# Performance work log

Hardware: AMD Instinct MI355X
Metric: run time of the kernel (lower is better)

## Reference

```python
import jax, jax.numpy as jnp
import numpy as np

N_EXPERTS = 8
TOP_K = 2

def setup_inputs() -> dict:
    key = jax.random.key(0)
    k1, k2, k3, k4 = jax.random.split(key, 4)
    B, T, C, F, E = 4, 1024, 1024, 2048, N_EXPERTS
    x = jax.random.normal(k1, (B, T, C), dtype=jnp.float32)
    router_w = jax.random.normal(k2, (E, C), dtype=jnp.float32) * 0.02
    w_v = jax.random.normal(k3, (E, C, 2 * F), dtype=jnp.float32) * 0.02
    c_proj = jax.random.normal(k4, (E, F, C), dtype=jnp.float32) * 0.02
    return {"x": x, "router_w": router_w, "w_v": w_v, "c_proj": c_proj}

def reference(x, router_w, w_v, c_proj):
    B, T, C = x.shape
    E = router_w.shape[0]
    # Router: top-k softmax
    logits = jnp.einsum('btc,ec->bte', x, router_w)
    probs = jax.nn.softmax(logits, axis=-1)
    weights, indices = jax.lax.top_k(probs, TOP_K)          # [B,T,K]
    weights = weights / jnp.sum(weights, axis=-1, keepdims=True)
    avg_probs = jnp.mean(probs, axis=(0, 1))
    aux_loss = E * jnp.sum(avg_probs * avg_probs)
    # Dense per-expert SwiGLU MLP on all tokens (idiomatic jax MoE reference)
    xf = x.reshape(B * T, C)                                # [N,C]
    h = jnp.einsum('nc,ecf->enf', xf, w_v)                  # [E,N,2F]
    gate, value = jnp.split(h, 2, axis=-1)
    act = jax.nn.silu(gate) * value                         # [E,N,F]
    eo = jnp.einsum('enf,efc->nec', act, c_proj)            # [N,E,C]
    # Combine: gather each token's top-k expert outputs and weight-sum
    idx = indices.reshape(B * T, TOP_K)                     # [N,K]
    w = weights.reshape(B * T, TOP_K)                       # [N,K]
    sel = jnp.take_along_axis(eo, idx[:, :, None], axis=1)  # [N,K,C]
    out = jnp.sum(w[:, :, None] * sel, axis=1)              # [N,C]
    return out.reshape(B, T, C), aux_loss
```

## Files before the change

kernel.cpp:

```cpp
#include <hip/hip_runtime.h>
#include <hip/hip_bf16.h>
#include <stdint.h>

#define N_TOK 4096
#define C_DIM 1024
#define F_DIM 2048
#define E_NUM 8
#define SMAX 9216
#define TILES_MAX 72
#define RBLK 1024

typedef __attribute__((ext_vector_type(4))) float f32x4;
typedef __attribute__((ext_vector_type(8))) short s16x8;

__device__ __forceinline__ uint16_t f2bf(float f) {
    unsigned x;
    __builtin_memcpy(&x, &f, 4);
    unsigned r = (x + 0x7fffu + ((x >> 16) & 1u)) >> 16;
    return (uint16_t)r;
}
__device__ __forceinline__ float bf2f(uint16_t u) {
    unsigned v = (unsigned)u << 16;
    float f;
    __builtin_memcpy(&f, &v, 4);
    return f;
}

#define GLL16(gp, lp)                                                                  \
    __builtin_amdgcn_global_load_lds((const __attribute__((address_space(1))) unsigned int*)(gp), \
                                     (__attribute__((address_space(3))) unsigned int*)(lp), 16, 0, 0)

__global__ void router_kernel(const float* __restrict__ x, const float* __restrict__ rw,
                              int* __restrict__ topk_idx, float* __restrict__ topk_w,
                              float* __restrict__ psum_part, int* __restrict__ cnt_part) {
    __shared__ float s_p[E_NUM];
    __shared__ int s_c[E_NUM];
    if (threadIdx.x < E_NUM) { s_p[threadIdx.x] = 0.f; s_c[threadIdx.x] = 0; }
    __syncthreads();

    int lane = threadIdx.x & 63;
    int wv = threadIdx.x >> 6;
    int t = blockIdx.x * 4 + wv;

    const float* xr = x + (size_t)t * C_DIM + lane * 16;
    float xs[16];
    for (int i = 0; i < 4; i++) *(float4*)&xs[i * 4] = *(const float4*)(xr + i * 4);

    float acc[E_NUM];
    for (int e = 0; e < E_NUM; e++) {
        const float* wr = rw + e * C_DIM + lane * 16;
        float s = 0.f;
        for (int i = 0; i < 4; i++) {
            float4 v = *(const float4*)(wr + i * 4);
            s += xs[i * 4] * v.x + xs[i * 4 + 1] * v.y + xs[i * 4 + 2] * v.z + xs[i * 4 + 3] * v.w;
        }
        acc[e] = s;
    }
    for (int off = 32; off > 0; off >>= 1)
        for (int e = 0; e < E_NUM; e++) acc[e] += __shfl_down(acc[e], off, 64);

    if (lane == 0) {
        float m = acc[0];
        for (int e = 1; e < E_NUM; e++) m = fmaxf(m, acc[e]);
        float p[E_NUM], s = 0.f;
        for (int e = 0; e < E_NUM; e++) { p[e] = __expf(acc[e] - m); s += p[e]; }
        float inv = 1.f / s;
        for (int e = 0; e < E_NUM; e++) { p[e] *= inv; atomicAdd(&s_p[e], p[e]); }
        int i0 = 0;
        for (int e = 1; e < E_NUM; e++) if (p[e] > p[i0]) i0 = e;
        int i1 = (i0 == 0) ? 1 : 0;
        for (int e = 0; e < E_NUM; e++) if (e != i0 && p[e] > p[i1]) i1 = e;
        float w0 = p[i0], w1 = p[i1], wsum = w0 + w1;
        topk_idx[t * 2] = i0; topk_idx[t * 2 + 1] = i1;
        topk_w[t * 2] = w0 / wsum; topk_w[t * 2 + 1] = w1 / wsum;
        atomicAdd(&s_c[i0], 1); atomicAdd(&s_c[i1], 1);
    }
    __syncthreads();
    if (threadIdx.x < E_NUM) {
        psum_part[blockIdx.x * E_NUM + threadIdx.x] = s_p[threadIdx.x];
        cnt_part[blockIdx.x * E_NUM + threadIdx.x] = s_c[threadIdx.x];
    }
}

__global__ void reduce_plan_kernel(const float* __restrict__ psum_part, const int* __restrict__ cnt_part,
                                   int* __restrict__ offsets, int* __restrict__ tile_expert,
                                   int* __restrict__ tile_row0, float* __restrict__ aux_out) {
    __shared__ float sp[256];
    __shared__ int sc[256];
    __shared__ int s_count[E_NUM];
    __shared__ float s_psum[E_NUM];
    int e = threadIdx.x >> 5, i = threadIdx.x & 31;
    float fp = 0.f; int c = 0;
    for (int j = i; j < RBLK; j += 32) { fp += psum_part[j * E_NUM + e]; c += cnt_part[j * E_NUM + e]; }
    sp[threadIdx.x] = fp; sc[threadIdx.x] = c;
    __syncthreads();
    for (int s = 16; s > 0; s >>= 1) {
        if (i < s) { sp[threadIdx.x] += sp[threadIdx.x + s]; sc[threadIdx.x] += sc[threadIdx.x + s]; }
        __syncthreads();
    }
    if (i == 0) { s_count[e] = sc[threadIdx.x]; s_psum[e] = sp[threadIdx.x]; }
    __syncthreads();
    if (threadIdx.x == 0) {
        int off = 0, t = 0;
        for (int ee = 0; ee < E_NUM; ee++) {
            offsets[ee] = off;
            int n = s_count[ee];
            int nt = (n + 127) >> 7;
            for (int k = 0; k < nt; k++) { tile_expert[t] = ee; tile_row0[t] = off + k * 128; t++; }
            off += nt * 128;
        }
        offsets[E_NUM] = off;
        for (; t < TILES_MAX; t++) tile_expert[t] = -1;
        float s = 0.f;
        for (int ee = 0; ee < E_NUM; ee++) { float a = s_psum[ee] * (1.f / N_TOK); s += a * a; }
        aux_out[0] = 8.f * s;
    }
}

__global__ void assign_kernel(const int* __restrict__ topk_idx, const float* __restrict__ topk_w,
                              const int* __restrict__ offsets, int* __restrict__ count2,
                              int* __restrict__ slot_map, float* __restrict__ slot_w,
                              int* __restrict__ tok_slot) {
    __shared__ int h[E_NUM];
    __shared__ int base[E_NUM];
    if (threadIdx.x < E_NUM) h[threadIdx.x] = 0;
    __syncthreads();
    int item = blockIdx.x * 256 + threadIdx.x;
    int e = topk_idx[item];
    int rank = atomicAdd(&h[e], 1);
    __syncthreads();
    if (threadIdx.x < E_NUM)
        base[threadIdx.x] = offsets[threadIdx.x] + atomicAdd(&count2[threadIdx.x], h[threadIdx.x]);
    __syncthreads();
    int slot = base[e] + rank;
    slot_map[slot] = item;
    slot_w[slot] = topk_w[item];
    tok_slot[item] = slot;
}

__global__ void gather_kernel(const float* __restrict__ x, const int* __restrict__ slot_map,
                              uint16_t* __restrict__ x_slots) {
    int slot = blockIdx.x;
    int item = slot_map[slot];
    if (item < 0) return;
    int t = item >> 1;
    float4 v = *(const float4*)(x + (size_t)t * C_DIM + threadIdx.x * 4);
    union { uint16_t u[4]; uint2 q; } r;
    r.u[0] = f2bf(v.x); r.u[1] = f2bf(v.y); r.u[2] = f2bf(v.z); r.u[3] = f2bf(v.w);
    *(uint2*)(x_slots + (size_t)slot * C_DIM + threadIdx.x * 4) = r.q;
}

__global__ __launch_bounds__(256) void convT_kernel(const float* __restrict__ in,
                                                    uint16_t* __restrict__ out, int R, int Cc) {
    __shared__ uint16_t s[128 * 66];
    size_t zb = (size_t)blockIdx.z * (size_t)R * Cc;
    int c0 = blockIdx.x * 64, r0 = blockIdx.y * 128;
    int cx = (threadIdx.x & 15) * 4, ry = threadIdx.x >> 4;
    for (int j = 0; j < 8; j++) {
        int r = ry + j * 16;
        float4 v = *(const float4*)(in + zb + (size_t)(r0 + r) * Cc + c0 + cx);
        uint16_t* p = &s[r * 66 + cx];
        p[0] = f2bf(v.x); p[1] = f2bf(v.y); p[2] = f2bf(v.z); p[3] = f2bf(v.w);
    }
    __syncthreads();
    int oc = threadIdx.x & 63, wseg = threadIdx.x >> 6;
    uint16_t tmp[32];
    for (int j = 0; j < 32; j++) tmp[j] = s[(wseg * 32 + j) * 66 + oc];
    uint4* dst = (uint4*)(out + zb + (size_t)(c0 + oc) * R + r0 + wseg * 32);
    dst[0] = *(const uint4*)&tmp[0];
    dst[1] = *(const uint4*)&tmp[8];
    dst[2] = *(const uint4*)&tmp[16];
    dst[3] = *(const uint4*)&tmp[24];
}


__global__ __launch_bounds__(256) void gemm1_kernel(const uint16_t* __restrict__ x_slots,
                                                    const uint16_t* __restrict__ wvT,
                                                    const int* __restrict__ tile_expert,
                                                    const int* __restrict__ tile_row0,
                                                    uint16_t* __restrict__ act) {
    int e = tile_expert[blockIdx.y];
    if (e < 0) return;
    int row0 = tile_row0[blockIdx.y];
    int j = blockIdx.x;
    __shared__ uint16_t As[128 * 32];
    __shared__ uint16_t Bg[64 * 32];
    __shared__ uint16_t Bv[64 * 32];
    int lane = threadIdx.x & 63, w = threadIdx.x >> 6;
    int wm = w & 1, wn = w >> 1;
    const uint16_t* wvb = wvT + (size_t)e * 4096 * 1024;

    int sk = (((lane & 3) ^ ((lane >> 3) & 3))) * 8;
    int ar = w * 32 + (lane >> 2);
    const uint16_t* agp0 = x_slots + (size_t)(row0 + ar) * C_DIM + sk;
    const uint16_t* agp1 = agp0 + (size_t)16 * C_DIM;
    int br = w * 16 + (lane >> 2);
    const uint16_t* bgp = wvb + (size_t)(j * 64 + br) * C_DIM + sk;
    const uint16_t* bvp = wvb + (size_t)(2048 + j * 64 + br) * C_DIM + sk;

    int cswz = ((lane >> 4) ^ ((lane >> 1) & 3)) * 8;

    f32x4 accg[4][2], accv[4][2];
    f32x4 z4 = {0.f, 0.f, 0.f, 0.f};
    for (int mf = 0; mf < 4; mf++)
        for (int nf = 0; nf < 2; nf++) { accg[mf][nf] = z4; accv[mf][nf] = z4; }

    for (int kt = 0; kt < 32; ++kt) {
        int ko = kt * 32;
        __syncthreads();
        GLL16(agp0 + ko, As + w * 1024);
        GLL16(agp1 + ko, As + w * 1024 + 512);
        GLL16(bgp + ko, Bg + w * 512);
        GLL16(bvp + ko, Bv + w * 512);
        __syncthreads();
        s16x8 af[4], bg[2], bv[2];
        for (int mf = 0; mf < 4; mf++)
            af[mf] = *(const s16x8*)&As[(wm * 64 + mf * 16 + (lane & 15)) * 32 + cswz];
        for (int nf = 0; nf < 2; nf++) {
            bg[nf] = *(const s16x8*)&Bg[(wn * 32 + nf * 16 + (lane & 15)) * 32 + cswz];
            bv[nf] = *(const s16x8*)&Bv[(wn * 32 + nf * 16 + (lane & 15)) * 32 + cswz];
        }
        for (int mf = 0; mf < 4; mf++)
            for (int nf = 0; nf < 2; nf++) {
                accg[mf][nf] = __builtin_amdgcn_mfma_f32_16x16x32_bf16(af[mf], bg[nf], accg[mf][nf], 0, 0, 0);
                accv[mf][nf] = __builtin_amdgcn_mfma_f32_16x16x32_bf16(af[mf], bv[nf], accv[mf][nf], 0, 0, 0);
            }
    }
    for (int mf = 0; mf < 4; mf++)
        for (int nf = 0; nf < 2; nf++)
            for (int r = 0; r < 4; r++) {
                int row = row0 + wm * 64 + mf * 16 + (lane >> 4) * 4 + r;
                int col = j * 64 + wn * 32 + nf * 16 + (lane & 15);
                float g = accg[mf][nf][r], v = accv[mf][nf][r];
                float a = g * v / (1.f + __expf(-g));
                act[(size_t)row * F_DIM + col] = f2bf(a);
            }
}

__global__ __launch_bounds__(256) void gemm2_kernel(const uint16_t* __restrict__ act,
                                                    const uint16_t* __restrict__ cpT,
                                                    const int* __restrict__ tile_expert,
                                                    const int* __restrict__ tile_row0,
                                                    const int* __restrict__ slot_map,
                                                    const float* __restrict__ slot_w,
                                                    uint16_t* __restrict__ eo) {
    int e = tile_expert[blockIdx.y];
    if (e < 0) return;
    int row0 = tile_row0[blockIdx.y];
    int cb = blockIdx.x * 128;
    __shared__ uint16_t As[128 * 32];
    __shared__ uint16_t Bs[128 * 32];
    int lane = threadIdx.x & 63, w = threadIdx.x >> 6;
    int wm = w & 1, wn = w >> 1;
    const uint16_t* cpb = cpT + (size_t)e * 1024 * 2048;

    int sk = (((lane & 3) ^ ((lane >> 3) & 3))) * 8;
    int ar = w * 32 + (lane >> 2);
    const uint16_t* agp0 = act + (size_t)(row0 + ar) * F_DIM + sk;
    const uint16_t* agp1 = agp0 + (size_t)16 * F_DIM;
    const uint16_t* bgp0 = cpb + (size_t)(cb + ar) * F_DIM + sk;
    const uint16_t* bgp1 = bgp0 + (size_t)16 * F_DIM;

    int cswz = ((lane >> 4) ^ ((lane >> 1) & 3)) * 8;

    f32x4 acc[4][4];
    f32x4 z4 = {0.f, 0.f, 0.f, 0.f};
    for (int mf = 0; mf < 4; mf++)
        for (int nf = 0; nf < 4; nf++) acc[mf][nf] = z4;

    for (int kt = 0; kt < 64; ++kt) {
        int ko = kt * 32;
        __syncthreads();
        GLL16(agp0 + ko, As + w * 1024);
        GLL16(agp1 + ko, As + w * 1024 + 512);
        GLL16(bgp0 + ko, Bs + w * 1024);
        GLL16(bgp1 + ko, Bs + w * 1024 + 512);
        __syncthreads();
        s16x8 af[4], bf[4];
        for (int mf = 0; mf < 4; mf++)
            af[mf] = *(const s16x8*)&As[(wm * 64 + mf * 16 + (lane & 15)) * 32 + cswz];
        for (int nf = 0; nf < 4; nf++)
            bf[nf] = *(const s16x8*)&Bs[(wn * 64 + nf * 16 + (lane & 15)) * 32 + cswz];
        for (int mf = 0; mf < 4; mf++)
            for (int nf = 0; nf < 4; nf++)
                acc[mf][nf] = __builtin_amdgcn_mfma_f32_16x16x32_bf16(af[mf], bf[nf], acc[mf][nf], 0, 0, 0);
    }
    for (int mf = 0; mf < 4; mf++)
        for (int r = 0; r < 4; r++) {
            int slotr = row0 + wm * 64 + mf * 16 + (lane >> 4) * 4 + r;
            int t2k = slot_map[slotr];
            if (t2k < 0) continue;
            float wgt = slot_w[slotr];
            for (int nf = 0; nf < 4; nf++) {
                int col = cb + wn * 64 + nf * 16 + (lane & 15);
                eo[(size_t)slotr * C_DIM + col] = f2bf(wgt * acc[mf][nf][r]);
            }
        }
}

__global__ void combine_kernel(const uint16_t* __restrict__ eo, const int* __restrict__ tok_slot,
                               float* __restrict__ out) {
    int t = blockIdx.x;
    int s0 = tok_slot[2 * t], s1 = tok_slot[2 * t + 1];
    int c = threadIdx.x * 4;
    uint2 a = *(const uint2*)(eo + (size_t)s0 * C_DIM + c);
    uint2 b = *(const uint2*)(eo + (size_t)s1 * C_DIM + c);
    float4 o;
    o.x = bf2f((uint16_t)(a.x & 0xffff)) + bf2f((uint16_t)(b.x & 0xffff));
    o.y = bf2f((uint16_t)(a.x >> 16)) + bf2f((uint16_t)(b.x >> 16));
    o.z = bf2f((uint16_t)(a.y & 0xffff)) + bf2f((uint16_t)(b.y & 0xffff));
    o.w = bf2f((uint16_t)(a.y >> 16)) + bf2f((uint16_t)(b.y >> 16));
    *(float4*)(out + (size_t)t * C_DIM + c) = o;
}

extern "C" void kernel_launch(void* const* d_in, const int* in_sizes, int n_in,
                              void* d_out, int out_size, void* d_ws, size_t ws_size,
                              hipStream_t stream) {
    (void)in_sizes; (void)n_in; (void)out_size; (void)ws_size;
    const float* x = (const float*)d_in[0];
    const float* rw = (const float*)d_in[1];
    const float* wv = (const float*)d_in[2];
    const float* cp = (const float*)d_in[3];
    float* out = (float*)d_out;

    char* ws = (char*)d_ws;
    size_t off = 0;
    auto alloc = [&](size_t sz) -> void* {
        off = (off + 255) & ~(size_t)255;
        void* p = ws + off;
        off += sz;
        return p;
    };
    uint16_t* wvT = (uint16_t*)alloc((size_t)E_NUM * 4096 * 1024 * 2);
    uint16_t* cpT = (uint16_t*)alloc((size_t)E_NUM * 1024 * 2048 * 2);
    uint16_t* x_slots = (uint16_t*)alloc((size_t)SMAX * C_DIM * 2);
    uint16_t* act = (uint16_t*)alloc((size_t)SMAX * F_DIM * 2);
    uint16_t* eo = (uint16_t*)alloc((size_t)SMAX * C_DIM * 2);
    float* psum_part = (float*)alloc((size_t)RBLK * E_NUM * 4);
    int* cnt_part = (int*)alloc((size_t)RBLK * E_NUM * 4);
    int* count2 = (int*)alloc(E_NUM * 4);
    int* offsets = (int*)alloc((E_NUM + 1) * 4);
    int* tile_expert = (int*)alloc(TILES_MAX * 4);
    int* tile_row0 = (int*)alloc(TILES_MAX * 4);
    int* topk_idx = (int*)alloc((size_t)N_TOK * 2 * 4);
    float* topk_w = (float*)alloc((size_t)N_TOK * 2 * 4);
    int* slot_map = (int*)alloc((size_t)SMAX * 4);
    float* slot_w = (float*)alloc((size_t)SMAX * 4);
    int* tok_slot = (int*)alloc((size_t)N_TOK * 2 * 4);

    hipMemsetAsync(count2, 0, E_NUM * 4, stream);
    hipMemsetAsync(slot_map, 0xFF, (size_t)SMAX * 4, stream);

    router_kernel<<<RBLK, 256, 0, stream>>>(x, rw, topk_idx, topk_w, psum_part, cnt_part);
    reduce_plan_kernel<<<1, 256, 0, stream>>>(psum_part, cnt_part, offsets, tile_expert, tile_row0,
                                              out + (size_t)N_TOK * C_DIM);
    assign_kernel<<<N_TOK * 2 / 256, 256, 0, stream>>>(topk_idx, topk_w, offsets, count2,
                                                       slot_map, slot_w, tok_slot);
    gather_kernel<<<SMAX, 256, 0, stream>>>(x, slot_map, x_slots);
    convT_kernel<<<dim3(4096 / 64, 1024 / 128, E_NUM), 256, 0, stream>>>(wv, wvT, 1024, 4096);
    convT_kernel<<<dim3(1024 / 64, 2048 / 128, E_NUM), 256, 0, stream>>>(cp, cpT, 2048, 1024);
    gemm1_kernel<<<dim3(32, TILES_MAX), 256, 0, stream>>>(x_slots, wvT, tile_expert, tile_row0, act);
    gemm2_kernel<<<dim3(8, TILES_MAX), 256, 0, stream>>>(act, cpT, tile_expert, tile_row0,
                                                         slot_map, slot_w, eo);
    combine_kernel<<<N_TOK, 256, 0, stream>>>(eo, tok_slot, out);
}
```

Before: 482.8 us.

## Double GEMM N-tiles to raise per-block reuse and halve grids; widen convT stores

gemm1 now computes 128 gate and 128 value columns per block instead of 64, and gemm2 computes 256 output columns instead of 128. This doubles accumulator work per wave and halves the grid width, so each A tile loaded into LDS feeds more MFMAs and A-matrix reloads drop. The convT store phase now uses 128 threads writing 64-element rows instead of 256 threads writing 32. The costs are many more accumulator registers (gemm1 goes to 128 floats of accumulators, gemm2 to 128), more LDS per block, and fewer blocks, which may cut occupancy or cause spills.

```diff
diff --git a/kernel.cpp b/kernel.cpp
--- a/kernel.cpp
+++ b/kernel.cpp
@@ -163,14 +163,13 @@
         p[0] = f2bf(v.x); p[1] = f2bf(v.y); p[2] = f2bf(v.z); p[3] = f2bf(v.w);
     }
     __syncthreads();
-    int oc = threadIdx.x & 63, wseg = threadIdx.x >> 6;
-    uint16_t tmp[32];
-    for (int j = 0; j < 32; j++) tmp[j] = s[(wseg * 32 + j) * 66 + oc];
-    uint4* dst = (uint4*)(out + zb + (size_t)(c0 + oc) * R + r0 + wseg * 32);
-    dst[0] = *(const uint4*)&tmp[0];
-    dst[1] = *(const uint4*)&tmp[8];
-    dst[2] = *(const uint4*)&tmp[16];
-    dst[3] = *(const uint4*)&tmp[24];
+    if (threadIdx.x < 128) {
+        int oc = threadIdx.x & 63, seg = threadIdx.x >> 6;
+        uint16_t tmp[64];
+        for (int j = 0; j < 64; j++) tmp[j] = s[(seg * 64 + j) * 66 + oc];
+        uint4* dst = (uint4*)(out + zb + (size_t)(c0 + oc) * R + r0 + seg * 64);
+        for (int q = 0; q < 8; q++) dst[q] = *(const uint4*)&tmp[q * 8];
+    }
 }
 
 
@@ -184,8 +183,8 @@
     int row0 = tile_row0[blockIdx.y];
     int j = blockIdx.x;
     __shared__ uint16_t As[128 * 32];
-    __shared__ uint16_t Bg[64 * 32];
-    __shared__ uint16_t Bv[64 * 32];
+    __shared__ uint16_t Bg[128 * 32];
+    __shared__ uint16_t Bv[128 * 32];
     int lane = threadIdx.x & 63, w = threadIdx.x >> 6;
     int wm = w & 1, wn = w >> 1;
     const uint16_t* wvb = wvT + (size_t)e * 4096 * 1024;
@@ -194,43 +193,46 @@
     int ar = w * 32 + (lane >> 2);
     const uint16_t* agp0 = x_slots + (size_t)(row0 + ar) * C_DIM + sk;
     const uint16_t* agp1 = agp0 + (size_t)16 * C_DIM;
-    int br = w * 16 + (lane >> 2);
-    const uint16_t* bgp = wvb + (size_t)(j * 64 + br) * C_DIM + sk;
-    const uint16_t* bvp = wvb + (size_t)(2048 + j * 64 + br) * C_DIM + sk;
+    const uint16_t* bgp0 = wvb + (size_t)(j * 128 + ar) * C_DIM + sk;
+    const uint16_t* bgp1 = bgp0 + (size_t)16 * C_DIM;
+    const uint16_t* bvp0 = wvb + (size_t)(2048 + j * 128 + ar) * C_DIM + sk;
+    const uint16_t* bvp1 = bvp0 + (size_t)16 * C_DIM;
 
     int cswz = ((lane >> 4) ^ ((lane >> 1) & 3)) * 8;
 
-    f32x4 accg[4][2], accv[4][2];
+    f32x4 accg[4][4], accv[4][4];
     f32x4 z4 = {0.f, 0.f, 0.f, 0.f};
     for (int mf = 0; mf < 4; mf++)
-        for (int nf = 0; nf < 2; nf++) { accg[mf][nf] = z4; accv[mf][nf] = z4; }
+        for (int nf = 0; nf < 4; nf++) { accg[mf][nf] = z4; accv[mf][nf] = z4; }
 
     for (int kt = 0; kt < 32; ++kt) {
         int ko = kt * 32;
         __syncthreads();
         GLL16(agp0 + ko, As + w * 1024);
         GLL16(agp1 + ko, As + w * 1024 + 512);
-        GLL16(bgp + ko, Bg + w * 512);
-        GLL16(bvp + ko, Bv + w * 512);
-        __syncthreads();
-        s16x8 af[4], bg[2], bv[2];
+        GLL16(bgp0 + ko, Bg + w * 1024);
+        GLL16(bgp1 + ko, Bg + w * 1024 + 512);
+        GLL16(bvp0 + ko, Bv + w * 1024);
+        GLL16(bvp1 + ko, Bv + w * 1024 + 512);
+        __syncthreads();
+        s16x8 af[4], bg[4], bv[4];
         for (int mf = 0; mf < 4; mf++)
             af[mf] = *(const s16x8*)&As[(wm * 64 + mf * 16 + (lane & 15)) * 32 + cswz];
-        for (int nf = 0; nf < 2; nf++) {
-            bg[nf] = *(const s16x8*)&Bg[(wn * 32 + nf * 16 + (lane & 15)) * 32 + cswz];
-            bv[nf] = *(const s16x8*)&Bv[(wn * 32 + nf * 16 + (lane & 15)) * 32 + cswz];
+        for (int nf = 0; nf < 4; nf++) {
+            bg[nf] = *(const s16x8*)&Bg[(wn * 64 + nf * 16 + (lane & 15)) * 32 + cswz];
+            bv[nf] = *(const s16x8*)&Bv[(wn * 64 + nf * 16 + (lane & 15)) * 32 + cswz];
         }
         for (int mf = 0; mf < 4; mf++)
-            for (int nf = 0; nf < 2; nf++) {
+            for (int nf = 0; nf < 4; nf++) {
                 accg[mf][nf] = __builtin_amdgcn_mfma_f32_16x16x32_bf16(af[mf], bg[nf], accg[mf][nf], 0, 0, 0);
                 accv[mf][nf] = __builtin_amdgcn_mfma_f32_16x16x32_bf16(af[mf], bv[nf], accv[mf][nf], 0, 0, 0);
             }
     }
     for (int mf = 0; mf < 4; mf++)
-        for (int nf = 0; nf < 2; nf++)
+        for (int nf = 0; nf < 4; nf++)
             for (int r = 0; r < 4; r++) {
                 int row = row0 + wm * 64 + mf * 16 + (lane >> 4) * 4 + r;
-                int col = j * 64 + wn * 32 + nf * 16 + (lane & 15);
+                int col = j * 128 + wn * 64 + nf * 16 + (lane & 15);
                 float g = accg[mf][nf][r], v = accv[mf][nf][r];
                 float a = g * v / (1.f + __expf(-g));
                 act[(size_t)row * F_DIM + col] = f2bf(a);
@@ -247,9 +249,9 @@
     int e = tile_expert[blockIdx.y];
     if (e < 0) return;
     int row0 = tile_row0[blockIdx.y];
-    int cb = blockIdx.x * 128;
+    int cb = blockIdx.x * 256;
     __shared__ uint16_t As[128 * 32];
-    __shared__ uint16_t Bs[128 * 32];
+    __shared__ uint16_t Bs[256 * 32];
     int lane = threadIdx.x & 63, w = threadIdx.x >> 6;
     int wm = w & 1, wn = w >> 1;
     const uint16_t* cpb = cpT + (size_t)e * 1024 * 2048;
@@ -258,31 +260,36 @@
     int ar = w * 32 + (lane >> 2);
     const uint16_t* agp0 = act + (size_t)(row0 + ar) * F_DIM + sk;
     const uint16_t* agp1 = agp0 + (size_t)16 * F_DIM;
-    const uint16_t* bgp0 = cpb + (size_t)(cb + ar) * F_DIM + sk;
+    int br = w * 64 + (lane >> 2);
+    const uint16_t* bgp0 = cpb + (size_t)(cb + br) * F_DIM + sk;
     const uint16_t* bgp1 = bgp0 + (size_t)16 * F_DIM;
+    const uint16_t* bgp2 = bgp0 + (size_t)32 * F_DIM;
+    const uint16_t* bgp3 = bgp0 + (size_t)48 * F_DIM;
 
     int cswz = ((lane >> 4) ^ ((lane >> 1) & 3)) * 8;
 
-    f32x4 acc[4][4];
+    f32x4 acc[4][8];
     f32x4 z4 = {0.f, 0.f, 0.f, 0.f};
     for (int mf = 0; mf < 4; mf++)
-        for (int nf = 0; nf < 4; nf++) acc[mf][nf] = z4;
+        for (int nf = 0; nf < 8; nf++) acc[mf][nf] = z4;
 
     for (int kt = 0; kt < 64; ++kt) {
         int ko = kt * 32;
         __syncthreads();
         GLL16(agp0 + ko, As + w * 1024);
         GLL16(agp1 + ko, As + w * 1024 + 512);
-        GLL16(bgp0 + ko, Bs + w * 1024);
-        GLL16(bgp1 + ko, Bs + w * 1024 + 512);
-        __syncthreads();
-        s16x8 af[4], bf[4];
+        GLL16(bgp0 + ko, Bs + w * 2048);
+        GLL16(bgp1 + ko, Bs + w * 2048 + 512);
+        GLL16(bgp2 + ko, Bs + w * 2048 + 1024);
+        GLL16(bgp3 + ko, Bs + w * 2048 + 1536);
+        __syncthreads();
+        s16x8 af[4], bf[8];
         for (int mf = 0; mf < 4; mf++)
             af[mf] = *(const s16x8*)&As[(wm * 64 + mf * 16 + (lane & 15)) * 32 + cswz];
-        for (int nf = 0; nf < 4; nf++)
-            bf[nf] = *(const s16x8*)&Bs[(wn * 64 + nf * 16 + (lane & 15)) * 32 + cswz];
+        for (int nf = 0; nf < 8; nf++)
+            bf[nf] = *(const s16x8*)&Bs[(wn * 128 + nf * 16 + (lane & 15)) * 32 + cswz];
         for (int mf = 0; mf < 4; mf++)
-            for (int nf = 0; nf < 4; nf++)
+            for (int nf = 0; nf < 8; nf++)
                 acc[mf][nf] = __builtin_amdgcn_mfma_f32_16x16x32_bf16(af[mf], bf[nf], acc[mf][nf], 0, 0, 0);
     }
     for (int mf = 0; mf < 4; mf++)
@@ -291,8 +298,8 @@
             int t2k = slot_map[slotr];
             if (t2k < 0) continue;
             float wgt = slot_w[slotr];
-            for (int nf = 0; nf < 4; nf++) {
-                int col = cb + wn * 64 + nf * 16 + (lane & 15);
+            for (int nf = 0; nf < 8; nf++) {
+                int col = cb + wn * 128 + nf * 16 + (lane & 15);
                 eo[(size_t)slotr * C_DIM + col] = f2bf(wgt * acc[mf][nf][r]);
             }
         }
@@ -359,8 +366,8 @@
     gather_kernel<<<SMAX, 256, 0, stream>>>(x, slot_map, x_slots);
     convT_kernel<<<dim3(4096 / 64, 1024 / 128, E_NUM), 256, 0, stream>>>(wv, wvT, 1024, 4096);
     convT_kernel<<<dim3(1024 / 64, 2048 / 128, E_NUM), 256, 0, stream>>>(cp, cpT, 2048, 1024);
-    gemm1_kernel<<<dim3(32, TILES_MAX), 256, 0, stream>>>(x_slots, wvT, tile_expert, tile_row0, act);
-    gemm2_kernel<<<dim3(8, TILES_MAX), 256, 0, stream>>>(act, cpT, tile_expert, tile_row0,
+    gemm1_kernel<<<dim3(16, TILES_MAX), 256, 0, stream>>>(x_slots, wvT, tile_expert, tile_row0, act);
+    gemm2_kernel<<<dim3(4, TILES_MAX), 256, 0, stream>>>(act, cpT, tile_expert, tile_row0,
                                                          slot_map, slot_w, eo);
     combine_kernel<<<N_TOK, 256, 0, stream>>>(eo, tok_slot, out);
 }
```

Result: slower. 649.2 us (+34.5%).
